# Kernel optimization log

Hardware: AMD Instinct MI355X
Metric: run time of the kernel (lower is better)

Reference implementation:

```python
import jax, jax.numpy as jnp
import numpy as np

MC, IN_C, OUT_C, K, STRIDE, PAD = 10, 16, 32, 3, 2, 1
D = IN_C * K * K  # 144


def setup_inputs() -> dict:
    key = jax.random.key(0)
    k1, k2 = jax.random.split(key)
    x = jax.random.normal(k1, (8, IN_C, 128, 128), dtype=jnp.float32)
    theta_logsigma = jnp.zeros((1,), jnp.float32)
    Omega_mean = jnp.zeros((D, OUT_C), jnp.float32)
    # init: theta_llscale * -2 = -log(in*k*k)
    Omega_logsigma = jnp.full((D, OUT_C), -np.log(float(D)), jnp.float32)
    Omega_eps = jax.random.normal(k2, (MC, D, OUT_C), dtype=jnp.float32)
    return {"x": x, "theta_logsigma": theta_logsigma, "Omega_mean": Omega_mean,
            "Omega_logsigma": Omega_logsigma, "Omega_eps": Omega_eps}


def reference(x, theta_logsigma, Omega_mean, Omega_logsigma, Omega_eps):
    B, _, H, W = x.shape
    # reparameterized weights: [mc, D, out]
    Omega = Omega_eps * jnp.exp(Omega_logsigma * 0.5) + Omega_mean
    # torch: view(mc,k,k,in,out).permute(0,4,3,1,2).reshape(mc*out,in,k,k)
    w = Omega.reshape(MC, K, K, IN_C, OUT_C).transpose(0, 4, 3, 1, 2)
    w = w.reshape(MC * OUT_C, IN_C, K, K)
    # F0 path: replicate x over mc -> [B, mc*in, H, W]
    xr = jnp.broadcast_to(x[None], (MC, B, IN_C, H, W)).transpose(1, 0, 2, 3, 4)
    xr = xr.reshape(B, MC * IN_C, H, W)
    phi_half = jax.lax.conv_general_dilated(
        xr, w, window_strides=(STRIDE, STRIDE),
        padding=[(PAD, PAD), (PAD, PAD)],
        dimension_numbers=("NCHW", "OIHW", "NCHW"),
        feature_group_count=MC)
    hw = phi_half.shape[-1]
    N_rf = OUT_C * hw * hw
    scale = jnp.exp(0.5 * theta_logsigma[0]) / jnp.sqrt(jnp.asarray(N_rf, x.dtype))
    ph = phi_half.reshape(B, MC, OUT_C, hw, hw)
    phi = jnp.concatenate([scale * jnp.cos(ph), scale * jnp.sin(ph)], axis=2)
    return phi.reshape(B, MC * 2 * OUT_C, hw, hw)
```

## Files before the change

kernel.cpp:

```cpp
#include <hip/hip_runtime.h>
#include <hip/hip_bf16.h>
#include <math.h>

#define MC_    10
#define IN_C_  16
#define OUT_C_ 32
#define K_     3
#define D_     144
#define KP_    160
#define H_     128
#define W_     128
#define HW_    64
#define B_     8

typedef __attribute__((ext_vector_type(8))) short short8;
typedef __attribute__((ext_vector_type(4))) float f32x4;

static __device__ __forceinline__ unsigned short f2bf(float v) {
    union { float f; unsigned u; } x; x.f = v;
    unsigned r = x.u + 0x7fff + ((x.u >> 16) & 1);
    return (unsigned short)(r >> 16);
}

__global__ __launch_bounds__(256) void prep_w_kernel(
    const float* __restrict__ eps, const float* __restrict__ logsig,
    const float* __restrict__ mean, unsigned short* __restrict__ w2)
{
    int i = blockIdx.x * 256 + threadIdx.x;
    if (i >= MC_ * OUT_C_ * KP_) return;
    int k  = i % KP_;
    int oc = (i / KP_) % OUT_C_;
    int mc = i / (KP_ * OUT_C_);
    float val = 0.0f;
    if (k < D_) {
        int doc = k * OUT_C_ + oc;
        val = eps[mc * (D_ * OUT_C_) + doc] * __expf(0.5f * logsig[doc]) + mean[doc];
    }
    w2[i] = f2bf(val);
}

__global__ __launch_bounds__(256) void conv_rff_mfma(
    const float* __restrict__ x,
    const unsigned short* __restrict__ w2,
    const float* __restrict__ theta,
    float* __restrict__ out)
{
    __shared__ __align__(16) unsigned short Alds[32 * 168];

    const int tid  = threadIdx.x;
    const int tile = blockIdx.x;
    const int b    = blockIdx.y;
    const int oh   = tile >> 1;
    const int ow0  = (tile & 1) << 5;
    const float* __restrict__ xb = x + (size_t)b * (IN_C_ * H_ * W_);

#pragma unroll
    for (int j = 0; j < 20; ++j) {
        int idx = j * 256 + tid;
        int m = idx & 31;
        int k = idx >> 5;
        float val = 0.0f;
        if (k < D_) {
            int ic = k & 15;
            int t  = k >> 4;
            int kh = (t * 11) >> 5;
            int kw = t - kh * 3;
            int ih = oh * 2 - 1 + kh;
            int iw = (ow0 + m) * 2 - 1 + kw;
            if ((unsigned)ih < (unsigned)H_ && (unsigned)iw < (unsigned)W_)
                val = xb[ic * (H_ * W_) + ih * W_ + iw];
        }
        Alds[m * 168 + k] = f2bf(val);
    }
    __syncthreads();

    const int lane  = tid & 63;
    const int wave  = tid >> 6;
    const int wn_oc = (wave & 1) << 4;
    const int wm_px = (wave >> 1) << 4;
    const int l15   = lane & 15;
    const int quad  = lane >> 4;

    short8 pf[5];
#pragma unroll
    for (int ks = 0; ks < 5; ++ks)
        pf[ks] = *(const short8*)&Alds[(wm_px + l15) * 168 + ks * 32 + quad * 8];

    const float scale = __expf(0.5f * theta[0]) * rsqrtf((float)(OUT_C_ * HW_ * HW_));

    float* __restrict__ po =
        out + (size_t)b * (MC_ * 2 * OUT_C_ * HW_ * HW_) + oh * HW_ + ow0 + wm_px + l15;

    for (int mc = 0; mc < MC_; ++mc) {
        const unsigned short* __restrict__ wmc = w2 + (size_t)mc * (OUT_C_ * KP_);
        short8 wf[5];
#pragma unroll
        for (int ks = 0; ks < 5; ++ks)
            wf[ks] = *(const short8*)&wmc[(wn_oc + l15) * KP_ + ks * 32 + quad * 8];

        f32x4 acc = {0.f, 0.f, 0.f, 0.f};
#pragma unroll
        for (int ks = 0; ks < 5; ++ks)
            acc = __builtin_amdgcn_mfma_f32_16x16x32_bf16(wf[ks], pf[ks], acc, 0, 0, 0);

        const int ch0 = mc * (2 * OUT_C_) + wn_oc + quad * 4;
#pragma unroll
        for (int r = 0; r < 4; ++r) {
            float s, c;
            __sincosf(acc[r], &s, &c);
            po[(size_t)(ch0 + r) * (HW_ * HW_)]           = scale * c;
            po[(size_t)(ch0 + r + OUT_C_) * (HW_ * HW_)]  = scale * s;
        }
    }
}

extern "C" void kernel_launch(void* const* d_in, const int* in_sizes, int n_in,
                              void* d_out, int out_size, void* d_ws, size_t ws_size,
                              hipStream_t stream)
{
    const float* x      = (const float*)d_in[0];
    const float* theta  = (const float*)d_in[1];
    const float* mean   = (const float*)d_in[2];
    const float* logsig = (const float*)d_in[3];
    const float* eps    = (const float*)d_in[4];
    float* out = (float*)d_out;
    unsigned short* W2 = (unsigned short*)d_ws;

    const int n_w = MC_ * OUT_C_ * KP_;
    prep_w_kernel<<<(n_w + 255) / 256, 256, 0, stream>>>(eps, logsig, mean, W2);

    dim3 grid(128, B_);
    conv_rff_mfma<<<grid, 256, 0, stream>>>(x, W2, theta, out);
}
```

Before: 112.6 us.

## Split MC loop across grid z-dimension and batch input gathers before LDS stores

```diff
diff --git a/kernel.cpp b/kernel.cpp
--- a/kernel.cpp
+++ b/kernel.cpp
@@ -12,6 +12,8 @@
 #define W_     128
 #define HW_    64
 #define B_     8
+#define MCG_   2
+#define NMCG_  (MC_ / MCG_)
 
 typedef __attribute__((ext_vector_type(8))) short short8;
 typedef __attribute__((ext_vector_type(4))) float f32x4;
@@ -50,10 +52,12 @@
     const int tid  = threadIdx.x;
     const int tile = blockIdx.x;
     const int b    = blockIdx.y;
+    const int mc0  = blockIdx.z * MCG_;
     const int oh   = tile >> 1;
     const int ow0  = (tile & 1) << 5;
     const float* __restrict__ xb = x + (size_t)b * (IN_C_ * H_ * W_);
 
+    float v[20];
 #pragma unroll
     for (int j = 0; j < 20; ++j) {
         int idx = j * 256 + tid;
@@ -70,7 +74,12 @@
             if ((unsigned)ih < (unsigned)H_ && (unsigned)iw < (unsigned)W_)
                 val = xb[ic * (H_ * W_) + ih * W_ + iw];
         }
-        Alds[m * 168 + k] = f2bf(val);
+        v[j] = val;
+    }
+#pragma unroll
+    for (int j = 0; j < 20; ++j) {
+        int idx = j * 256 + tid;
+        Alds[(idx & 31) * 168 + (idx >> 5)] = f2bf(v[j]);
     }
     __syncthreads();
 
@@ -86,24 +95,29 @@
     for (int ks = 0; ks < 5; ++ks)
         pf[ks] = *(const short8*)&Alds[(wm_px + l15) * 168 + ks * 32 + quad * 8];
 
+    short8 wf[MCG_][5];
+#pragma unroll
+    for (int g = 0; g < MCG_; ++g) {
+        const unsigned short* __restrict__ wmc =
+            w2 + (size_t)(mc0 + g) * (OUT_C_ * KP_);
+#pragma unroll
+        for (int ks = 0; ks < 5; ++ks)
+            wf[g][ks] = *(const short8*)&wmc[(wn_oc + l15) * KP_ + ks * 32 + quad * 8];
+    }
+
     const float scale = __expf(0.5f * theta[0]) * rsqrtf((float)(OUT_C_ * HW_ * HW_));
 
     float* __restrict__ po =
         out + (size_t)b * (MC_ * 2 * OUT_C_ * HW_ * HW_) + oh * HW_ + ow0 + wm_px + l15;
 
-    for (int mc = 0; mc < MC_; ++mc) {
-        const unsigned short* __restrict__ wmc = w2 + (size_t)mc * (OUT_C_ * KP_);
-        short8 wf[5];
 #pragma unroll
-        for (int ks = 0; ks < 5; ++ks)
-            wf[ks] = *(const short8*)&wmc[(wn_oc + l15) * KP_ + ks * 32 + quad * 8];
-
+    for (int g = 0; g < MCG_; ++g) {
         f32x4 acc = {0.f, 0.f, 0.f, 0.f};
 #pragma unroll
         for (int ks = 0; ks < 5; ++ks)
-            acc = __builtin_amdgcn_mfma_f32_16x16x32_bf16(wf[ks], pf[ks], acc, 0, 0, 0);
+            acc = __builtin_amdgcn_mfma_f32_16x16x32_bf16(wf[g][ks], pf[ks], acc, 0, 0, 0);
 
-        const int ch0 = mc * (2 * OUT_C_) + wn_oc + quad * 4;
+        const int ch0 = (mc0 + g) * (2 * OUT_C_) + wn_oc + quad * 4;
 #pragma unroll
         for (int r = 0; r < 4; ++r) {
             float s, c;
@@ -129,6 +143,6 @@
     const int n_w = MC_ * OUT_C_ * KP_;
     prep_w_kernel<<<(n_w + 255) / 256, 256, 0, stream>>>(eps, logsig, mean, W2);
 
-    dim3 grid(128, B_);
+    dim3 grid(128, B_, NMCG_);
     conv_rff_mfma<<<grid, 256, 0, stream>>>(x, W2, theta, out);
 }
```

New measurement: 120.9 us. 1.07x slower.

## Stage MFMA phases through LDS for float4 coalesced output stores, full-row tiles

Applied to the files above, without the earlier changes.

```diff
diff --git a/kernel.cpp b/kernel.cpp
--- a/kernel.cpp
+++ b/kernel.cpp
@@ -12,6 +12,7 @@
 #define W_     128
 #define HW_    64
 #define B_     8
+#define PSTR_  68
 
 typedef __attribute__((ext_vector_type(8))) short short8;
 typedef __attribute__((ext_vector_type(4))) float f32x4;
@@ -39,78 +40,91 @@
     w2[i] = f2bf(val);
 }
 
-__global__ __launch_bounds__(256) void conv_rff_mfma(
+__global__ __launch_bounds__(512) void conv_rff_mfma(
     const float* __restrict__ x,
     const unsigned short* __restrict__ w2,
     const float* __restrict__ theta,
     float* __restrict__ out)
 {
-    __shared__ __align__(16) unsigned short Alds[32 * 168];
+    __shared__ __align__(16) unsigned short Alds[64 * 168];
+    __shared__ __align__(16) float Phase[OUT_C_ * PSTR_];
 
-    const int tid  = threadIdx.x;
-    const int tile = blockIdx.x;
-    const int b    = blockIdx.y;
-    const int oh   = tile >> 1;
-    const int ow0  = (tile & 1) << 5;
+    const int tid = threadIdx.x;
+    const int oh  = blockIdx.x;
+    const int b   = blockIdx.y;
     const float* __restrict__ xb = x + (size_t)b * (IN_C_ * H_ * W_);
 
 #pragma unroll
-    for (int j = 0; j < 20; ++j) {
-        int idx = j * 256 + tid;
-        int m = idx & 31;
-        int k = idx >> 5;
+    for (int j = 0; j < 18; ++j) {
+        int idx = j * 512 + tid;
+        int m = idx & 63;
+        int k = idx >> 6;
+        int ic = k & 15;
+        int t  = k >> 4;
+        int kh = (t * 11) >> 5;
+        int kw = t - kh * 3;
+        int ih = oh * 2 - 1 + kh;
+        int iw = m * 2 - 1 + kw;
         float val = 0.0f;
-        if (k < D_) {
-            int ic = k & 15;
-            int t  = k >> 4;
-            int kh = (t * 11) >> 5;
-            int kw = t - kh * 3;
-            int ih = oh * 2 - 1 + kh;
-            int iw = (ow0 + m) * 2 - 1 + kw;
-            if ((unsigned)ih < (unsigned)H_ && (unsigned)iw < (unsigned)W_)
-                val = xb[ic * (H_ * W_) + ih * W_ + iw];
-        }
+        if ((unsigned)ih < (unsigned)H_ && (unsigned)iw < (unsigned)W_)
+            val = xb[ic * (H_ * W_) + ih * W_ + iw];
         Alds[m * 168 + k] = f2bf(val);
+    }
+#pragma unroll
+    for (int j = 0; j < 2; ++j) {
+        int idx = j * 512 + tid;
+        Alds[(idx & 63) * 168 + 144 + (idx >> 6)] = 0;
     }
     __syncthreads();
 
-    const int lane  = tid & 63;
-    const int wave  = tid >> 6;
-    const int wn_oc = (wave & 1) << 4;
-    const int wm_px = (wave >> 1) << 4;
-    const int l15   = lane & 15;
-    const int quad  = lane >> 4;
+    const int lane = tid & 63;
+    const int wave = tid >> 6;
+    const int h    = wave & 1;
+    const int q    = wave >> 1;
+    const int l15  = lane & 15;
+    const int quad = lane >> 4;
 
     short8 pf[5];
 #pragma unroll
     for (int ks = 0; ks < 5; ++ks)
-        pf[ks] = *(const short8*)&Alds[(wm_px + l15) * 168 + ks * 32 + quad * 8];
+        pf[ks] = *(const short8*)&Alds[(q * 16 + l15) * 168 + ks * 32 + quad * 8];
 
     const float scale = __expf(0.5f * theta[0]) * rsqrtf((float)(OUT_C_ * HW_ * HW_));
 
+    const int oc_w = tid >> 4;
+    const int px0  = (tid & 15) << 2;
     float* __restrict__ po =
-        out + (size_t)b * (MC_ * 2 * OUT_C_ * HW_ * HW_) + oh * HW_ + ow0 + wm_px + l15;
+        out + (size_t)b * (MC_ * 2 * OUT_C_ * HW_ * HW_) + oh * HW_ + px0;
 
     for (int mc = 0; mc < MC_; ++mc) {
         const unsigned short* __restrict__ wmc = w2 + (size_t)mc * (OUT_C_ * KP_);
         short8 wf[5];
 #pragma unroll
         for (int ks = 0; ks < 5; ++ks)
-            wf[ks] = *(const short8*)&wmc[(wn_oc + l15) * KP_ + ks * 32 + quad * 8];
+            wf[ks] = *(const short8*)&wmc[(h * 16 + l15) * KP_ + ks * 32 + quad * 8];
 
         f32x4 acc = {0.f, 0.f, 0.f, 0.f};
 #pragma unroll
         for (int ks = 0; ks < 5; ++ks)
             acc = __builtin_amdgcn_mfma_f32_16x16x32_bf16(wf[ks], pf[ks], acc, 0, 0, 0);
 
-        const int ch0 = mc * (2 * OUT_C_) + wn_oc + quad * 4;
+        __syncthreads();
 #pragma unroll
-        for (int r = 0; r < 4; ++r) {
-            float s, c;
-            __sincosf(acc[r], &s, &c);
-            po[(size_t)(ch0 + r) * (HW_ * HW_)]           = scale * c;
-            po[(size_t)(ch0 + r + OUT_C_) * (HW_ * HW_)]  = scale * s;
-        }
+        for (int r = 0; r < 4; ++r)
+            Phase[(h * 16 + quad * 4 + r) * PSTR_ + q * 16 + l15] = acc[r];
+        __syncthreads();
+
+        float4 ph = *(const float4*)&Phase[oc_w * PSTR_ + px0];
+        float4 cv, sv;
+        __sincosf(ph.x, &sv.x, &cv.x);
+        __sincosf(ph.y, &sv.y, &cv.y);
+        __sincosf(ph.z, &sv.z, &cv.z);
+        __sincosf(ph.w, &sv.w, &cv.w);
+        cv.x *= scale; cv.y *= scale; cv.z *= scale; cv.w *= scale;
+        sv.x *= scale; sv.y *= scale; sv.z *= scale; sv.w *= scale;
+        const size_t chc = (size_t)(mc * (2 * OUT_C_) + oc_w) * (HW_ * HW_);
+        *(float4*)(po + chc)                              = cv;
+        *(float4*)(po + chc + (size_t)OUT_C_ * HW_ * HW_) = sv;
     }
 }
 
@@ -129,6 +143,6 @@
     const int n_w = MC_ * OUT_C_ * KP_;
     prep_w_kernel<<<(n_w + 255) / 256, 256, 0, stream>>>(eps, logsig, mean, W2);
 
-    dim3 grid(128, B_);
-    conv_rff_mfma<<<grid, 256, 0, stream>>>(x, W2, theta, out);
+    dim3 grid(HW_, B_);
+    conv_rff_mfma<<<grid, 512, 0, stream>>>(x, W2, theta, out);
 }
```

Measured after the change: 113.2 us. Within noise of the previous version (+0.5%).
